# Kernel tuning notes

Measured on AMD Instinct MI355X. Metric: run time of the kernel, lower is better.

## Reference

```python
import jax, jax.numpy as jnp
import numpy as np

N, D, K, P, A = 16384, 256, 32, 64, 5
H, KD, NPT, FACT = 8, 32, 8, 2
RBF_BINS, RBF_MAX, REL_CLIP = 16, 10.0, 32


def _norm(v, eps=1e-6):
    return v * jax.lax.rsqrt(jnp.square(v).sum(-1, keepdims=True) + eps)


def extract_frames(pos):
    # pos: [N, A, 3]; backbone atoms 0=N, 1=CA, 2=C (Gram-Schmidt AF-style frame)
    n, ca, c = pos[:, 0], pos[:, 1], pos[:, 2]
    e1 = _norm(c - ca)
    u = n - ca
    e2 = _norm(u - (u * e1).sum(-1, keepdims=True) * e1)
    e3 = jnp.cross(e1, e2)
    R = jnp.stack([e1, e2, e3], axis=-1)  # [N,3,3], columns = frame axes
    t = ca
    local = jnp.einsum('nji,naj->nai', R, pos - t[:, None])  # R^T (p - t)
    return R, t, local


def distance_rbf(d):
    centers = jnp.linspace(0.0, RBF_MAX, RBF_BINS)
    sigma = RBF_MAX / RBF_BINS
    return jnp.exp(-jnp.square((d[..., None] - centers) / sigma))


def layer_norm(x, scale, offset, eps=1e-5):
    mu = x.mean(-1, keepdims=True)
    var = jnp.square(x - mu).mean(-1, keepdims=True)
    return (x - mu) * jax.lax.rsqrt(var + eps) * scale + offset


def setup_inputs() -> dict:
    key = jax.random.key(0)
    ks = jax.random.split(key, 20)
    f32 = jnp.float32
    rnd = lambda i, shape, s=0.02: jax.random.normal(ks[i], shape, f32) * s
    inp = {}
    inp['local'] = jax.random.normal(ks[0], (N, D), f32)
    inp['pos'] = jax.random.normal(ks[1], (N, A, 3), f32) * 3.0
    inp['neighbours'] = jax.random.randint(ks[2], (N, K), 0, N, jnp.int32)
    inp['resi'] = jnp.arange(N, dtype=jnp.int32) % 512
    inp['chain'] = jnp.arange(N, dtype=jnp.int32) // 2048
    inp['batch'] = jnp.arange(N, dtype=jnp.int32) // 4096
    inp['update_mask'] = jnp.ones((N, 1), bool)
    inp['mask'] = jnp.ones((N,), bool)
    FIN = A * 3 + A * RBF_BINS
    FPAIR = A * 3 + A * RBF_BINS + (2 * REL_CLIP + 1) + 2
    FOUT = H * KD + H * P + H * NPT * 3 + H * NPT
    inp['w_in'] = rnd(3, (FIN, D))
    inp['w_pair'] = rnd(4, (FPAIR, P))
    inp['b_pair'] = jnp.zeros((P,), f32)
    inp['ln1_s'] = jnp.ones((D,), f32); inp['ln1_o'] = jnp.zeros((D,), f32)
    inp['wq'] = rnd(5, (D, H * KD)); inp['wk'] = rnd(6, (D, H * KD)); inp['wv'] = rnd(7, (D, H * KD))
    inp['wqp'] = rnd(8, (D, H * NPT * 3)); inp['wkp'] = rnd(9, (D, H * NPT * 3)); inp['wvp'] = rnd(10, (D, H * NPT * 3))
    inp['wb'] = rnd(11, (P, H))
    inp['gamma'] = jnp.ones((H,), f32)
    inp['wo'] = rnd(12, (FOUT, D)); inp['bo'] = jnp.zeros((D,), f32)
    inp['ln2_s'] = jnp.ones((D,), f32); inp['ln2_o'] = jnp.zeros((D,), f32)
    DH = D * FACT
    inp['wg'] = rnd(13, (D, DH)); inp['wvm'] = rnd(14, (D, DH)); inp['wom'] = rnd(15, (DH, D))
    inp['ln3_s'] = jnp.ones((D,), f32); inp['ln3_o'] = jnp.zeros((D,), f32)
    inp['wpos'] = rnd(16, (D, A * 3))
    return inp


def reference(local, pos, w_in, w_pair, b_pair, ln1_s, ln1_o, wq, wk, wv, wqp, wkp, wvp,
              wb, gamma, wo, bo, ln2_s, ln2_o, wg, wvm, wom, ln3_s, ln3_o, wpos,
              neighbours, resi, chain, batch, update_mask, mask):
    n_res = local.shape[0]
    kk = neighbours.shape[1]
    R, t, local_pos = extract_frames(pos)  # [N,3,3], [N,3], [N,A,3]
    # --- geometric input features ---
    dloc = jnp.sqrt(jnp.square(local_pos).sum(-1) + 1e-12)
    feat = jnp.concatenate([_norm(local_pos).reshape(n_res, -1),
                            distance_rbf(dloc).reshape(n_res, -1)], axis=-1)
    local = local + feat @ w_in
    # --- pair features over kNN edges ---
    idx = jnp.clip(neighbours, 0, n_res - 1)
    pos_j = pos[idx]  # [N,K,A,3]
    rel = jnp.einsum('nji,nkaj->nkai', R, pos_j - t[:, None, None])  # neighbour atoms in frame i
    dij = jnp.sqrt(jnp.square(rel).sum(-1) + 1e-12)  # [N,K,A]
    dirs = rel / (dij[..., None] + 1e-6)
    rp = jnp.clip(resi[idx] - resi[:, None], -REL_CLIP, REL_CLIP) + REL_CLIP
    rp_oh = jax.nn.one_hot(rp, 2 * REL_CLIP + 1, dtype=local.dtype)
    same_chain = (chain[idx] == chain[:, None])[..., None].astype(local.dtype)
    same_batch = (batch[idx] == batch[:, None])[..., None].astype(local.dtype)
    pf = jnp.concatenate([dirs.reshape(n_res, kk, -1), distance_rbf(dij).reshape(n_res, kk, -1),
                          rp_oh, same_chain, same_batch], axis=-1)
    pair = jax.nn.gelu(pf @ w_pair + b_pair)  # [N,K,P]
    pair_mask = mask[:, None] & mask[idx] & (neighbours >= 0) & (batch[idx] == batch[:, None])
    # --- sparse invariant point attention ---
    x = layer_norm(local, ln1_s, ln1_o)
    q = (x @ wq).reshape(n_res, H, KD)
    k = (x @ wk).reshape(n_res, H, KD)
    v = (x @ wv).reshape(n_res, H, KD)
    to_glob = lambda pts: jnp.einsum('nij,nhpj->nhpi', R, pts) + t[:, None, None]
    qp = to_glob((x @ wqp).reshape(n_res, H, NPT, 3))
    kp = to_glob((x @ wkp).reshape(n_res, H, NPT, 3))
    vp = to_glob((x @ wvp).reshape(n_res, H, NPT, 3))
    qk = jnp.einsum('nhd,nkhd->nkh', q, k[idx]) / np.float32(np.sqrt(KD))
    d2 = jnp.square(qp[:, None] - kp[idx]).sum(-1).sum(-1)  # [N,K,H]
    wc = np.float32(np.sqrt(2.0 / (9.0 * NPT)))
    wl = np.float32(np.sqrt(1.0 / 3.0))
    logits = wl * (qk + pair @ wb - 0.5 * wc * jax.nn.softplus(gamma) * d2)
    logits = jnp.where(pair_mask[..., None], logits, -1e9)
    att = jax.nn.softmax(logits, axis=1)
    att = jnp.where(pair_mask[..., None], att, 0.0)
    o_s = jnp.einsum('nkh,nkhd->nhd', att, v[idx]).reshape(n_res, -1)
    o_pt = jnp.einsum('nkh,nkhpi->nhpi', att, vp[idx])
    o_pt = jnp.einsum('nji,nhpj->nhpi', R, o_pt - t[:, None, None])  # back to local frame
    o_n = jnp.sqrt(jnp.square(o_pt).sum(-1) + 1e-8)
    o_pr = jnp.einsum('nkh,nkc->nhc', att, pair).reshape(n_res, -1)
    ipa = jnp.concatenate([o_s, o_pr, o_pt.reshape(n_res, -1), o_n.reshape(n_res, -1)], -1) @ wo + bo
    local = local + ipa
    # --- gated MLP ---
    x = layer_norm(local, ln2_s, ln2_o)
    local = local + (jax.nn.gelu(x @ wg) * (x @ wvm)) @ wom
    # --- equivariant position update (scale = 1.0) ---
    x = layer_norm(local, ln3_s, ln3_o)
    new_lp = local_pos + (x @ wpos).reshape(n_res, A, 3)
    new_pos = jnp.einsum('nij,naj->nai', R, new_lp) + t[:, None]
    pos = jnp.where(update_mask[..., None], new_pos, pos)
    return local, pos
```

## Files before the change

### kernel.cpp

```cpp
#include <hip/hip_runtime.h>
#include <hip/hip_bf16.h>
#include <math.h>

#define DMODEL 256
#define KNB 32
#define NHEAD 8
#define FIN 95
#define FPD 95
#define KPAD 104
#define FOUT 1024
#define DHID 512
#define BTS 36
#define PRS 72

typedef __hip_bfloat16 bf16;
typedef __attribute__((ext_vector_type(8))) short short8;
typedef __attribute__((ext_vector_type(4))) float floatx4;

__device__ inline float B2F(bf16 x) { return __bfloat162float(x); }
__device__ inline bf16 F2B(float x) { return __float2bfloat16(x); }
__device__ inline unsigned short f2bs(float x) {
    bf16 h = __float2bfloat16(x);
    return *reinterpret_cast<unsigned short*>(&h);
}
__device__ inline float bs2f(short s) {
    return __uint_as_float(((unsigned)(unsigned short)s) << 16);
}

__device__ inline float gelu_t(float x) {
    return 0.5f * x * (1.f + tanhf(0.7978845608028654f * (x + 0.044715f * x * x * x)));
}

__device__ inline float gelu_f(float x) {
    float u = 1.5957691216057308f * x * (1.f + 0.044715f * x * x);
    float t = 1.f - 2.f / (1.f + __expf(u));
    return 0.5f * x * (1.f + t);
}

#define OFF_WALL 0
#define OFF_WO   344064
#define OFF_WG   606208
#define OFF_WVM  737280
#define OFF_WOM  868352
#define OFF_WP   999424
#define OFF_WIN  1006080
#define OFF_WBM  1032704
#define WT_TOTAL 1033728

__global__ __launch_bounds__(256) void kT(const float* __restrict__ wq, const float* __restrict__ wk,
                                          const float* __restrict__ wv, const float* __restrict__ wqp,
                                          const float* __restrict__ wkp, const float* __restrict__ wvp,
                                          const float* __restrict__ wo, const float* __restrict__ wg,
                                          const float* __restrict__ wvm, const float* __restrict__ wom,
                                          const float* __restrict__ w_pair, const float* __restrict__ w_in,
                                          const float* __restrict__ wbm,
                                          unsigned short* __restrict__ wt) {
    int stride = gridDim.x * 256;
    for (int e = blockIdx.x * 256 + threadIdx.x; e < WT_TOTAL; e += stride) {
        float v;
        if (e < OFF_WO) {
            int n = e >> 8, k = e & 255;
            if (n < 256) v = wq[k * 256 + n];
            else if (n < 512) v = wk[k * 256 + n - 256];
            else if (n < 768) v = wv[k * 256 + n - 512];
            else if (n < 960) v = wqp[k * 192 + n - 768];
            else if (n < 1152) v = wkp[k * 192 + n - 960];
            else v = wvp[k * 192 + n - 1152];
        } else if (e < OFF_WG) {
            int u = e - OFF_WO; int n = u >> 10, k = u & 1023;
            v = wo[k * 256 + n];
        } else if (e < OFF_WVM) {
            int u = e - OFF_WG; int n = u >> 8, k = u & 255;
            v = wg[k * 512 + n];
        } else if (e < OFF_WOM) {
            int u = e - OFF_WVM; int n = u >> 8, k = u & 255;
            v = wvm[k * 512 + n];
        } else if (e < OFF_WP) {
            int u = e - OFF_WOM; int n = u >> 9, k = u & 511;
            v = wom[k * 256 + n];
        } else if (e < OFF_WIN) {
            int u = e - OFF_WP; int n = u / KPAD, k = u % KPAD;
            v = (k < FPD) ? w_pair[k * 64 + n] : 0.f;
        } else if (e < OFF_WBM) {
            int u = e - OFF_WIN; int n = u / KPAD, k = u % KPAD;
            v = (k < FIN) ? w_in[k * 256 + n] : 0.f;
        } else {
            int u = e - OFF_WBM; int n = u >> 6, k = u & 63;
            v = (n < NHEAD) ? wbm[k * 8 + n] : 0.f;
        }
        wt[e] = f2bs(v);
    }
}

__global__ __launch_bounds__(256) void kA1(const float* __restrict__ pos,
                                           float* __restrict__ Rw,
                                           float* __restrict__ lpw,
                                           unsigned short* __restrict__ featb) {
    int tid = threadIdx.x;
    int res = tid >> 5, lt = tid & 31;
    int ri = blockIdx.x * 8 + res;
    const float* pp = pos + (size_t)ri * 15;
    float nx = pp[0], ny = pp[1], nz = pp[2];
    float cax = pp[3], cay = pp[4], caz = pp[5];
    float cx = pp[6], cy = pp[7], cz = pp[8];
    float e1x = cx - cax, e1y = cy - cay, e1z = cz - caz;
    float inv = rsqrtf(e1x * e1x + e1y * e1y + e1z * e1z + 1e-6f);
    e1x *= inv; e1y *= inv; e1z *= inv;
    float ux = nx - cax, uy = ny - cay, uz = nz - caz;
    float d = ux * e1x + uy * e1y + uz * e1z;
    float wx = ux - d * e1x, wy = uy - d * e1y, wz = uz - d * e1z;
    inv = rsqrtf(wx * wx + wy * wy + wz * wz + 1e-6f);
    float e2x = wx * inv, e2y = wy * inv, e2z = wz * inv;
    float e3x = e1y * e2z - e1z * e2y;
    float e3y = e1z * e2x - e1x * e2z;
    float e3z = e1x * e2y - e1y * e2x;
    float R[9] = {e1x, e2x, e3x, e1y, e2y, e3y, e1z, e2z, e3z};

    __shared__ float lpS[8][15];
    __shared__ float ddS[8][5], dinvS[8][5];

    if (lt < 9) Rw[(size_t)ri * 9 + lt] = R[lt];
    if (lt < 15) {
        int a = lt / 3, ii = lt % 3;
        float px = pp[a * 3 + 0] - cax, py = pp[a * 3 + 1] - cay, pz = pp[a * 3 + 2] - caz;
        float v = R[0 * 3 + ii] * px + R[1 * 3 + ii] * py + R[2 * 3 + ii] * pz;
        lpS[res][lt] = v;
        lpw[(size_t)ri * 15 + lt] = v;
    }
    __syncthreads();
    if (lt < 5) {
        float s = lpS[res][lt * 3] * lpS[res][lt * 3] + lpS[res][lt * 3 + 1] * lpS[res][lt * 3 + 1] +
                  lpS[res][lt * 3 + 2] * lpS[res][lt * 3 + 2];
        ddS[res][lt] = sqrtf(s + 1e-12f);
        dinvS[res][lt] = rsqrtf(s + 1e-6f);
    }
    __syncthreads();
    for (int e = lt; e < KPAD; e += 32) {
        float v;
        if (e < 15) v = lpS[res][e] * dinvS[res][e / 3];
        else if (e < 95) {
            int u = e - 15, a = u >> 4, b = u & 15;
            float z = (ddS[res][a] - (float)b * (10.f / 15.f)) * (1.f / 0.625f);
            v = expf(-z * z);
        } else v = 0.f;
        featb[(size_t)ri * KPAD + e] = f2bs(v);
    }
}

__global__ __launch_bounds__(256) void kB(const float* __restrict__ local,
                                          const unsigned short* __restrict__ featb,
                                          const float* __restrict__ ln1_s,
                                          const float* __restrict__ ln1_o,
                                          const unsigned short* __restrict__ wAllT,
                                          const unsigned short* __restrict__ w_inT,
                                          float* __restrict__ dlocal,
                                          bf16* __restrict__ qbh, bf16* __restrict__ kvb,
                                          bf16* __restrict__ qpl, bf16* __restrict__ kpl,
                                          bf16* __restrict__ vpl) {
    int r0 = blockIdx.x * 32;
    int tid = threadIdx.x;
    __shared__ __align__(16) unsigned short featA[32 * KPAD];
    __shared__ __align__(16) unsigned short xbf[32 * 264];
    __shared__ float statsS[32 * 4];

    {
        const short8* src = reinterpret_cast<const short8*>(featb + (size_t)r0 * KPAD);
        short8* dst = reinterpret_cast<short8*>(featA);
        for (int c = tid; c < 32 * KPAD / 8; c += 256) dst[c] = src[c];
    }
    __syncthreads();

    int lane = tid & 63, w = tid >> 6;
    int mtile = w & 1, par = w >> 1;
    int m = lane & 15, quad = lane >> 4;

    short8 fa[3];
#pragma unroll
    for (int ks = 0; ks < 3; ks++)
        fa[ks] = *reinterpret_cast<const short8*>(&featA[(mtile * 16 + m) * KPAD + ks * 32 + quad * 8]);
    float lupv[8][4];
#pragma unroll
    for (int j = 0; j < 8; j++) {
        int nt = par + 2 * j;
        floatx4 c = {0.f, 0.f, 0.f, 0.f};
        const short8* bp = reinterpret_cast<const short8*>(w_inT + (size_t)(nt * 16 + m) * KPAD);
#pragma unroll
        for (int ks = 0; ks < 3; ks++)
            c = __builtin_amdgcn_mfma_f32_16x16x32_bf16(fa[ks], bp[ks * 4 + quad], c, 0, 0, 0);
        int col = nt * 16 + m;
#pragma unroll
        for (int r = 0; r < 4; r++) {
            int row = mtile * 16 + quad * 4 + r;
            float lv = local[(size_t)(r0 + row) * 256 + col] + c[r];
            lupv[j][r] = lv;
            dlocal[(size_t)(r0 + row) * 256 + col] = lv;
        }
    }
    {
        float s[4] = {0.f, 0.f, 0.f, 0.f}, ss[4] = {0.f, 0.f, 0.f, 0.f};
#pragma unroll
        for (int j = 0; j < 8; j++)
#pragma unroll
            for (int r = 0; r < 4; r++) { s[r] += lupv[j][r]; ss[r] += lupv[j][r] * lupv[j][r]; }
#pragma unroll
        for (int mask = 1; mask < 16; mask <<= 1)
#pragma unroll
            for (int r = 0; r < 4; r++) { s[r] += __shfl_xor(s[r], mask); ss[r] += __shfl_xor(ss[r], mask); }
        if (m == 0) {
#pragma unroll
            for (int r = 0; r < 4; r++) {
                int row = mtile * 16 + quad * 4 + r;
                statsS[row * 4 + par * 2 + 0] = s[r];
                statsS[row * 4 + par * 2 + 1] = ss[r];
            }
        }
    }
    __syncthreads();
    {
        float mu[4], rs_[4];
#pragma unroll
        for (int r = 0; r < 4; r++) {
            int row = mtile * 16 + quad * 4 + r;
            float S = statsS[row * 4 + 0] + statsS[row * 4 + 2];
            float SS = statsS[row * 4 + 1] + statsS[row * 4 + 3];
            float m_ = S * (1.f / 256.f);
            mu[r] = m_;
            rs_[r] = rsqrtf(SS * (1.f / 256.f) - m_ * m_ + 1e-5f);
        }
#pragma unroll
        for (int j = 0; j < 8; j++) {
            int col = (par + 2 * j) * 16 + m;
            float g = ln1_s[col], o = ln1_o[col];
#pragma unroll
            for (int r = 0; r < 4; r++) {
                int row = mtile * 16 + quad * 4 + r;
                xbf[row * 264 + col] = f2bs((lupv[j][r] - mu[r]) * rs_[r] * g + o);
            }
        }
    }
    __syncthreads();

    short8 afr[8];
#pragma unroll
    for (int ks = 0; ks < 8; ks++)
        afr[ks] = *reinterpret_cast<const short8*>(&xbf[(mtile * 16 + m) * 264 + ks * 32 + quad * 8]);
    for (int nt = par; nt < 84; nt += 2) {
        floatx4 c = {0.f, 0.f, 0.f, 0.f};
        const short8* bp = reinterpret_cast<const short8*>(wAllT + (size_t)(nt * 16 + m) * 256);
#pragma unroll
        for (int ks = 0; ks < 8; ks++)
            c = __builtin_amdgcn_mfma_f32_16x16x32_bf16(afr[ks], bp[ks * 4 + quad], c, 0, 0, 0);
        int colg = nt * 16 + m;
        bf16* O; int c0, ncol;
        if (colg < 256)       { O = qbh; c0 = colg;        ncol = 256; }
        else if (colg < 768)  { O = kvb; c0 = colg - 256;  ncol = 512; }
        else if (colg < 960)  { O = qpl; c0 = colg - 768;  ncol = 192; }
        else if (colg < 1152) { O = kpl; c0 = colg - 960;  ncol = 192; }
        else                  { O = vpl; c0 = colg - 1152; ncol = 192; }
#pragma unroll
        for (int r = 0; r < 4; r++) {
            int rg = r0 + mtile * 16 + quad * 4 + r;
            O[(size_t)rg * ncol + c0] = F2B(c[r]);
        }
    }
}

__global__ __launch_bounds__(256) void kP(const bf16* __restrict__ qpl,
                                          const bf16* __restrict__ kpl,
                                          const bf16* __restrict__ vpl,
                                          const float* __restrict__ Rw,
                                          const float* __restrict__ pos,
                                          float* __restrict__ qpg,
                                          float* __restrict__ kvpg) {
    int r0 = blockIdx.x * 4;
    int tid = threadIdx.x;
    for (int u = tid; u < 4 * 192; u += 256) {
        int r = u / 192, e = u % 192, hp = e / 3, ii = e % 3;
        int ri = r0 + r;
        float R0 = Rw[(size_t)ri * 9 + ii * 3 + 0];
        float R1 = Rw[(size_t)ri * 9 + ii * 3 + 1];
        float R2 = Rw[(size_t)ri * 9 + ii * 3 + 2];
        float tt = pos[(size_t)ri * 15 + 3 + ii];
        size_t base = (size_t)ri * 192 + hp * 3;
        qpg[(size_t)ri * 192 + e] = R0 * B2F(qpl[base]) + R1 * B2F(qpl[base + 1]) + R2 * B2F(qpl[base + 2]) + tt;
        kvpg[(size_t)ri * 384 + e] = R0 * B2F(kpl[base]) + R1 * B2F(kpl[base + 1]) + R2 * B2F(kpl[base + 2]) + tt;
        kvpg[(size_t)ri * 384 + 192 + e] = R0 * B2F(vpl[base]) + R1 * B2F(vpl[base + 1]) + R2 * B2F(vpl[base + 2]) + tt;
    }
}

__global__ __launch_bounds__(256) void kC(const float* __restrict__ pos,
                                          const int* __restrict__ nbr,
                                          const int* __restrict__ resi,
                                          const int* __restrict__ chain,
                                          const int* __restrict__ batch,
                                          const int* __restrict__ mask,
                                          const float* __restrict__ Rw,
                                          const float* __restrict__ w_pair,
                                          const unsigned short* __restrict__ wT,
                                          const float* __restrict__ b_pair,
                                          const unsigned short* __restrict__ wbmT,
                                          const float* __restrict__ gamma,
                                          const bf16* __restrict__ qbh,
                                          const bf16* __restrict__ kvb,
                                          const float* __restrict__ qpg,
                                          const float* __restrict__ kvpg,
                                          bf16* __restrict__ ipab,
                                          int N) {
    int i = blockIdx.x;
    int tid = threadIdx.x;
    __shared__ __align__(16) unsigned short BigT[512 * BTS];
    __shared__ __align__(16) unsigned short pairR[32 * PRS];
    __shared__ __align__(16) unsigned short attb[16 * 40];
    __shared__ __align__(16) float qS[256];
    __shared__ __align__(16) float qpS[192];
    __shared__ __align__(16) float pbS[256];
    __shared__ float spS[NHEAD];
    __shared__ int anyS;
    __shared__ int idxS[KNB], rpS[KNB], scS[KNB], sbS[KNB], pmS[KNB];
    __shared__ __align__(16) union UShare {
        unsigned short pfA[32 * KPAD];
        struct { float ipaS[FOUT]; float optg[192]; } o;
    } uS;

    float R[9];
#pragma unroll
    for (int u = 0; u < 9; u++) R[u] = Rw[(size_t)i * 9 + u];
    float t0 = pos[(size_t)i * 15 + 3];
    float t1 = pos[(size_t)i * 15 + 4];
    float t2 = pos[(size_t)i * 15 + 5];

    qS[tid] = B2F(qbh[(size_t)i * 256 + tid]);
    if (tid < 192) qpS[tid] = qpg[(size_t)i * 192 + tid];
    if (tid < NHEAD) spS[tid] = log1pf(expf(gamma[tid]));
    if (tid < KNB) {
        int nb = nbr[(size_t)i * KNB + tid];
        int j = min(max(nb, 0), N - 1);
        idxS[tid] = j;
        int rp = resi[j] - resi[i];
        rp = min(max(rp, -32), 32) + 32;
        rpS[tid] = rp;
        scS[tid] = (chain[j] == chain[i]) ? 1 : 0;
        sbS[tid] = (batch[j] == batch[i]) ? 1 : 0;
        pmS[tid] = (mask[i] != 0 && mask[j] != 0 && nb >= 0 && batch[j] == batch[i]) ? 1 : 0;
    }
    __syncthreads();
    if (tid < 64) {
        unsigned long long b = __ballot((tid < KNB) && (pmS[tid] != 0));
        if (tid == 0) anyS = (b != 0ULL) ? 1 : 0;
    }
    if (tid < 160) {
        int kk = tid & 31, a = tid >> 5;
        int j = idxS[kk];
        const float* pj = pos + (size_t)j * 15 + a * 3;
        float px = pj[0] - t0, py = pj[1] - t1, pz = pj[2] - t2;
        float r0_ = R[0] * px + R[3] * py + R[6] * pz;
        float r1_ = R[1] * px + R[4] * py + R[7] * pz;
        float r2_ = R[2] * px + R[5] * py + R[8] * pz;
        float s = r0_ * r0_ + r1_ * r1_ + r2_ * r2_;
        float dij = sqrtf(s + 1e-12f);
        float di = 1.f / (dij + 1e-6f);
        uS.pfA[kk * KPAD + a * 3 + 0] = f2bs(r0_ * di);
        uS.pfA[kk * KPAD + a * 3 + 1] = f2bs(r1_ * di);
        uS.pfA[kk * KPAD + a * 3 + 2] = f2bs(r2_ * di);
        for (int b = 0; b < 16; b++) {
            float z = (dij - (float)b * (10.f / 15.f)) * (1.f / 0.625f);
            uS.pfA[kk * KPAD + 15 + a * 16 + b] = f2bs(__expf(-z * z));
        }
    }
    if (tid < KNB) uS.pfA[tid * KPAD + FPD] = 0;
    __syncthreads();

    {
        int lane = tid & 63;
        int wv = tid >> 6;
        int n0 = wv * 16;
        int mrow = lane & 15;
        int quad = lane >> 4;
        floatx4 c0 = {0.f, 0.f, 0.f, 0.f};
        floatx4 c1 = {0.f, 0.f, 0.f, 0.f};
#pragma unroll
        for (int ks = 0; ks < 3; ks++) {
            int k0 = ks * 32 + quad * 8;
            short8 a0 = *reinterpret_cast<const short8*>(&uS.pfA[mrow * KPAD + k0]);
            short8 a1 = *reinterpret_cast<const short8*>(&uS.pfA[(16 + mrow) * KPAD + k0]);
            short8 bb = *reinterpret_cast<const short8*>(&wT[(n0 + mrow) * KPAD + k0]);
            c0 = __builtin_amdgcn_mfma_f32_16x16x32_bf16(a0, bb, c0, 0, 0, 0);
            c1 = __builtin_amdgcn_mfma_f32_16x16x32_bf16(a1, bb, c1, 0, 0, 0);
        }
        int col = n0 + mrow;
        float bp = b_pair[col];
        float w160 = w_pair[160 * 64 + col];
        float w161 = w_pair[161 * 64 + col];
#pragma unroll
        for (int mt = 0; mt < 2; mt++) {
            floatx4 cc = mt ? c1 : c0;
#pragma unroll
            for (int r = 0; r < 4; r++) {
                int row = mt * 16 + quad * 4 + r;
                float s = cc[r] + bp + w_pair[(95 + rpS[row]) * 64 + col] +
                          (scS[row] ? w160 : 0.f) + (sbS[row] ? w161 : 0.f);
                unsigned short gb = f2bs(gelu_f(s));
                pairR[row * PRS + col] = gb;
                BigT[(448 + col) * BTS + row] = gb;
            }
        }
    }
    __syncthreads();

    {
        int kk = tid & 31, seg = tid >> 5;
        int j = idxS[kk];
        {
            const short8* src = reinterpret_cast<const short8*>(kvb + (size_t)j * 512 + 256 + seg * 32);
            short8 v0 = src[0], v1 = src[1], v2 = src[2], v3 = src[3];
#pragma unroll
            for (int c = 0; c < 8; c++) BigT[(seg * 32 + c) * BTS + kk] = (unsigned short)v0[c];
#pragma unroll
            for (int c = 0; c < 8; c++) BigT[(seg * 32 + 8 + c) * BTS + kk] = (unsigned short)v1[c];
#pragma unroll
            for (int c = 0; c < 8; c++) BigT[(seg * 32 + 16 + c) * BTS + kk] = (unsigned short)v2[c];
#pragma unroll
            for (int c = 0; c < 8; c++) BigT[(seg * 32 + 24 + c) * BTS + kk] = (unsigned short)v3[c];
        }
        {
            const floatx4* src = reinterpret_cast<const floatx4*>(kvpg + (size_t)j * 384 + 192 + seg * 24);
            floatx4 f[6];
#pragma unroll
            for (int g = 0; g < 6; g++) f[g] = src[g];
            float tv[3] = {t0, t1, t2};
#pragma unroll
            for (int g = 0; g < 6; g++)
#pragma unroll
                for (int c2 = 0; c2 < 4; c2++) {
                    int x = g * 4 + c2;
                    float val = f[g][c2] - tv[x % 3];
                    BigT[(256 + seg * 24 + x) * BTS + kk] = f2bs(val);
                }
        }
    }
    {
        int w = tid >> 6;
        if (w < 2) {
            int lane = tid & 63, la = lane & 15, quad = lane >> 4;
            floatx4 c = {0.f, 0.f, 0.f, 0.f};
#pragma unroll
            for (int ks = 0; ks < 2; ks++) {
                short8 a = *reinterpret_cast<const short8*>(&pairR[(w * 16 + la) * PRS + ks * 32 + quad * 8]);
                short8 b = *reinterpret_cast<const short8*>(wbmT + la * 64 + ks * 32 + quad * 8);
                c = __builtin_amdgcn_mfma_f32_16x16x32_bf16(a, b, c, 0, 0, 0);
            }
            if (la < NHEAD) {
#pragma unroll
                for (int r = 0; r < 4; r++)
                    pbS[(w * 16 + quad * 4 + r) * 8 + la] = c[r];
            }
        }
    }
    __syncthreads();

    {
        int kk = tid >> 3, h = tid & 7;
        int j = idxS[kk];
        float qk = 0.f;
        const short8* kj8 = reinterpret_cast<const short8*>(kvb + (size_t)j * 512 + h * 32);
        const floatx4* qh4 = reinterpret_cast<const floatx4*>(qS + h * 32);
#pragma unroll
        for (int e = 0; e < 4; e++) {
            short8 kv = kj8[e];
            floatx4 qa = qh4[2 * e], qb = qh4[2 * e + 1];
            qk += qa[0] * bs2f(kv[0]) + qa[1] * bs2f(kv[1]) + qa[2] * bs2f(kv[2]) + qa[3] * bs2f(kv[3]) +
                  qb[0] * bs2f(kv[4]) + qb[1] * bs2f(kv[5]) + qb[2] * bs2f(kv[6]) + qb[3] * bs2f(kv[7]);
        }
        qk *= 0.17677669529663687f;
        float d2 = 0.f;
        const floatx4* kp4 = reinterpret_cast<const floatx4*>(kvpg + (size_t)j * 384 + h * 24);
        const floatx4* qp4 = reinterpret_cast<const floatx4*>(qpS + h * 24);
#pragma unroll
        for (int e = 0; e < 6; e++) {
            floatx4 kv = kp4[e], qv = qp4[e];
#pragma unroll
            for (int q = 0; q < 4; q++) {
                float df = qv[q] - kv[q];
                d2 += df * df;
            }
        }
        float pb = pbS[kk * 8 + h];
        float lgt = 0.5773502691896258f * (qk + pb - (1.f / 12.f) * spS[h] * d2);
        pbS[kk * 8 + h] = pmS[kk] ? lgt : -1e9f;
    }
    __syncthreads();

    if (tid < 64) {
        int h = tid >> 3, sub = tid & 7;
        float m = -INFINITY;
        float lv[4];
#pragma unroll
        for (int q = 0; q < 4; q++) {
            lv[q] = pbS[(sub + 8 * q) * 8 + h];
            m = fmaxf(m, lv[q]);
        }
#pragma unroll
        for (int mk = 1; mk < 8; mk <<= 1) m = fmaxf(m, __shfl_xor(m, mk));
        float s = 0.f, ex[4];
#pragma unroll
        for (int q = 0; q < 4; q++) { ex[q] = __expf(lv[q] - m); s += ex[q]; }
#pragma unroll
        for (int mk = 1; mk < 8; mk <<= 1) s += __shfl_xor(s, mk);
        float invs = 1.f / s;
#pragma unroll
        for (int q = 0; q < 4; q++) {
            int kk = sub + 8 * q;
            float a = pmS[kk] ? ex[q] * invs : 0.f;
            attb[h * 40 + kk] = f2bs(a);
        }
    } else if (tid < 128) {
        int t2 = tid - 64;
        int h2 = 8 + (t2 >> 3);
        int k0 = (t2 & 7) * 4;
#pragma unroll
        for (int q = 0; q < 4; q++) attb[h2 * 40 + k0 + q] = 0;
    }
    __syncthreads();

    {
        int lane = tid & 63, w = tid >> 6;
        int la = lane & 15, quad = lane >> 4;
        short8 af = *reinterpret_cast<const short8*>(&attb[la * 40 + quad * 8]);
        float* oB = uS.o.ipaS;
#pragma unroll
        for (int n8 = 0; n8 < 8; n8++) {
            int nt = w * 8 + n8;
            int colg = nt * 16 + la;
            union { short8 s; unsigned long long u[2]; } bb;
            const unsigned long long* bp = reinterpret_cast<const unsigned long long*>(&BigT[colg * BTS + quad * 8]);
            bb.u[0] = bp[0]; bb.u[1] = bp[1];
            floatx4 z = {0.f, 0.f, 0.f, 0.f};
            floatx4 d = __builtin_amdgcn_mfma_f32_16x16x32_bf16(af, bb.s, z, 0, 0, 0);
            if (quad < 2) {
                if (colg < 448) {
                    int h_req, dst;
                    if (colg < 256) { h_req = colg >> 5; dst = (h_req << 5) + (colg & 31); }
                    else            { int e = colg - 256; h_req = e / 24; dst = 1024 + e; }
                    if ((h_req >> 2) == quad) {
#pragma unroll
                        for (int r = 0; r < 4; r++)
                            if ((h_req & 3) == r) oB[dst] = d[r];
                    }
                } else {
                    int c = colg - 448;
#pragma unroll
                    for (int r = 0; r < 4; r++)
                        oB[256 + (quad * 4 + r) * 64 + c] = d[r];
                }
            }
        }
    }
    __syncthreads();

    if (tid < 192) {
        int hp = tid / 3, ii = tid % 3;
        float corr = anyS ? 0.f : -1.f;
        const float* optg = uS.o.ipaS + 1024;
        float v0 = optg[hp * 3 + 0] + corr * t0;
        float v1 = optg[hp * 3 + 1] + corr * t1;
        float v2 = optg[hp * 3 + 2] + corr * t2;
        uS.o.ipaS[768 + tid] = R[0 + ii] * v0 + R[3 + ii] * v1 + R[6 + ii] * v2;
    }
    __syncthreads();
    if (tid < 64) {
        float a0 = uS.o.ipaS[768 + tid * 3], a1 = uS.o.ipaS[768 + tid * 3 + 1], a2 = uS.o.ipaS[768 + tid * 3 + 2];
        uS.o.ipaS[960 + tid] = sqrtf(a0 * a0 + a1 * a1 + a2 * a2 + 1e-8f);
    }
    __syncthreads();
    for (int u = tid; u < FOUT; u += 256) ipab[(size_t)i * FOUT + u] = F2B(uS.o.ipaS[u]);
}

__global__ __launch_bounds__(256) void kDE(const bf16* __restrict__ ipab,
                                           const unsigned short* __restrict__ woT,
                                           const float* __restrict__ bo,
                                           const float* __restrict__ ln2_s,
                                           const float* __restrict__ ln2_o,
                                           const unsigned short* __restrict__ wgT,
                                           const unsigned short* __restrict__ wvmT,
                                           const unsigned short* __restrict__ womT,
                                           float* __restrict__ dlocal) {
    int r0 = blockIdx.x * 32;
    int tid = threadIdx.x;
    __shared__ __align__(16) unsigned short xbf[32 * 264];
    __shared__ __align__(16) unsigned short hbf[32 * 520];
    __shared__ float statsS[32 * 4];
    int lane = tid & 63, w = tid >> 6;
    int mtile = w & 1, par = w >> 1, m = lane & 15, quad = lane >> 4;

    floatx4 l2[8];
#pragma unroll
    for (int j = 0; j < 8; j++) l2[j] = {0.f, 0.f, 0.f, 0.f};
    const short8* arow = reinterpret_cast<const short8*>(ipab + (size_t)(r0 + mtile * 16 + m) * 1024);
    for (int ks = 0; ks < 32; ks++) {
        short8 a = arow[ks * 4 + quad];
#pragma unroll
        for (int j = 0; j < 8; j++) {
            int nt = par + 2 * j;
            const short8* bp = reinterpret_cast<const short8*>(woT + (size_t)(nt * 16 + m) * 1024);
            l2[j] = __builtin_amdgcn_mfma_f32_16x16x32_bf16(a, bp[ks * 4 + quad], l2[j], 0, 0, 0);
        }
    }
#pragma unroll
    for (int j = 0; j < 8; j++) {
        int colg = (par + 2 * j) * 16 + m;
        float bov = bo[colg];
#pragma unroll
        for (int r = 0; r < 4; r++) {
            int row = mtile * 16 + quad * 4 + r;
            l2[j][r] += dlocal[(size_t)(r0 + row) * 256 + colg] + bov;
        }
    }
    {
        float s[4] = {0.f, 0.f, 0.f, 0.f}, ss[4] = {0.f, 0.f, 0.f, 0.f};
#pragma unroll
        for (int j = 0; j < 8; j++)
#pragma unroll
            for (int r = 0; r < 4; r++) { s[r] += l2[j][r]; ss[r] += l2[j][r] * l2[j][r]; }
#pragma unroll
        for (int mask = 1; mask < 16; mask <<= 1)
#pragma unroll
            for (int r = 0; r < 4; r++) { s[r] += __shfl_xor(s[r], mask); ss[r] += __shfl_xor(ss[r], mask); }
        if (m == 0) {
#pragma unroll
            for (int r = 0; r < 4; r++) {
                int row = mtile * 16 + quad * 4 + r;
                statsS[row * 4 + par * 2 + 0] = s[r];
                statsS[row * 4 + par * 2 + 1] = ss[r];
            }
        }
    }
    __syncthreads();
    {
        float mu[4], rs_[4];
#pragma unroll
        for (int r = 0; r < 4; r++) {
            int row = mtile * 16 + quad * 4 + r;
            float S = statsS[row * 4 + 0] + statsS[row * 4 + 2];
            float SS = statsS[row * 4 + 1] + statsS[row * 4 + 3];
            float m_ = S * (1.f / 256.f);
            mu[r] = m_;
            rs_[r] = rsqrtf(SS * (1.f / 256.f) - m_ * m_ + 1e-5f);
        }
#pragma unroll
        for (int j = 0; j < 8; j++) {
            int colg = (par + 2 * j) * 16 + m;
            float g = ln2_s[colg], o = ln2_o[colg];
#pragma unroll
            for (int r = 0; r < 4; r++) {
                int row = mtile * 16 + quad * 4 + r;
                xbf[row * 264 + colg] = f2bs((l2[j][r] - mu[r]) * rs_[r] * g + o);
            }
        }
    }
    __syncthreads();
    short8 afr[8];
#pragma unroll
    for (int ks = 0; ks < 8; ks++)
        afr[ks] = *reinterpret_cast<const short8*>(&xbf[(mtile * 16 + m) * 264 + ks * 32 + quad * 8]);
    for (int nt = par; nt < 32; nt += 2) {
        floatx4 cg = {0.f, 0.f, 0.f, 0.f};
        floatx4 cv = {0.f, 0.f, 0.f, 0.f};
        const short8* bg = reinterpret_cast<const short8*>(wgT + (size_t)(nt * 16 + m) * 256);
        const short8* bv = reinterpret_cast<const short8*>(wvmT + (size_t)(nt * 16 + m) * 256);
#pragma unroll
        for (int ks = 0; ks < 8; ks++) {
            cg = __builtin_amdgcn_mfma_f32_16x16x32_bf16(afr[ks], bg[ks * 4 + quad], cg, 0, 0, 0);
            cv = __builtin_amdgcn_mfma_f32_16x16x32_bf16(afr[ks], bv[ks * 4 + quad], cv, 0, 0, 0);
        }
#pragma unroll
        for (int r = 0; r < 4; r++) {
            int row = mtile * 16 + quad * 4 + r;
            hbf[row * 520 + nt * 16 + m] = f2bs(gelu_t(cg[r]) * cv[r]);
        }
    }
    __syncthreads();
    floatx4 acc[8];
#pragma unroll
    for (int j = 0; j < 8; j++) acc[j] = {0.f, 0.f, 0.f, 0.f};
    for (int ks = 0; ks < 16; ks++) {
        short8 a = *reinterpret_cast<const short8*>(&hbf[(mtile * 16 + m) * 520 + ks * 32 + quad * 8]);
#pragma unroll
        for (int j = 0; j < 8; j++) {
            int nt = par + 2 * j;
            const short8* bp = reinterpret_cast<const short8*>(womT + (size_t)(nt * 16 + m) * 512);
            acc[j] = __builtin_amdgcn_mfma_f32_16x16x32_bf16(a, bp[ks * 4 + quad], acc[j], 0, 0, 0);
        }
    }
#pragma unroll
    for (int j = 0; j < 8; j++) {
        int colg = (par + 2 * j) * 16 + m;
#pragma unroll
        for (int r = 0; r < 4; r++) {
            int row = mtile * 16 + quad * 4 + r;
            dlocal[(size_t)(r0 + row) * 256 + colg] = l2[j][r] + acc[j][r];
        }
    }
}

__global__ __launch_bounds__(256) void kF(const float* __restrict__ dlocal,
                                          const float* __restrict__ ln3_s,
                                          const float* __restrict__ ln3_o,
                                          const float* __restrict__ wpos,
                                          const float* __restrict__ lpw,
                                          const float* __restrict__ Rw,
                                          const float* __restrict__ pos,
                                          const int* __restrict__ umask,
                                          float* __restrict__ outp) {
    int tid = threadIdx.x;
    int r = tid >> 5, lt = tid & 31;
    int ri = blockIdx.x * 8 + r;
    __shared__ float x3S[8][256];
    __shared__ float nlS[8][15];
    {
        const floatx4* src = reinterpret_cast<const floatx4*>(dlocal + (size_t)ri * 256 + lt * 8);
        floatx4 v0 = src[0], v1 = src[1];
        float s = 0.f, ss = 0.f;
#pragma unroll
        for (int q = 0; q < 4; q++) {
            s += v0[q] + v1[q];
            ss += v0[q] * v0[q] + v1[q] * v1[q];
        }
#pragma unroll
        for (int mask = 1; mask < 32; mask <<= 1) { s += __shfl_xor(s, mask); ss += __shfl_xor(ss, mask); }
        float mu = s * (1.f / 256.f);
        float var = ss * (1.f / 256.f) - mu * mu;
        float rs = rsqrtf(var + 1e-5f);
#pragma unroll
        for (int q = 0; q < 4; q++) {
            int f0 = lt * 8 + q, f1 = lt * 8 + 4 + q;
            x3S[r][f0] = (v0[q] - mu) * rs * ln3_s[f0] + ln3_o[f0];
            x3S[r][f1] = (v1[q] - mu) * rs * ln3_s[f1] + ln3_o[f1];
        }
    }
    __syncthreads();
    {
        int g = tid >> 5, sub = tid & 31;
        for (int out = g; out < 120; out += 8) {
            int rr = out / 15, e = out % 15;
            float partial = 0.f;
#pragma unroll
            for (int i2 = 0; i2 < 8; i2++) {
                int f = sub + 32 * i2;
                partial += x3S[rr][f] * wpos[f * 15 + e];
            }
#pragma unroll
            for (int mask = 1; mask < 32; mask <<= 1) partial += __shfl_xor(partial, mask);
            if (sub == 0) nlS[rr][e] = lpw[(size_t)(blockIdx.x * 8 + rr) * 15 + e] + partial;
        }
    }
    __syncthreads();
    if (tid < 120) {
        int rr = tid / 15, e = tid % 15;
        int rj = blockIdx.x * 8 + rr;
        int a2 = e / 3, ii = e % 3;
        float R0 = Rw[(size_t)rj * 9 + ii * 3 + 0];
        float R1 = Rw[(size_t)rj * 9 + ii * 3 + 1];
        float R2 = Rw[(size_t)rj * 9 + ii * 3 + 2];
        float tt = pos[(size_t)rj * 15 + 3 + ii];
        float np = R0 * nlS[rr][a2 * 3 + 0] + R1 * nlS[rr][a2 * 3 + 1] + R2 * nlS[rr][a2 * 3 + 2] + tt;
        float old = pos[(size_t)rj * 15 + e];
        outp[(size_t)rj * 15 + e] = (umask[rj] != 0) ? np : old;
    }
}

extern "C" void kernel_launch(void* const* d_in, const int* in_sizes, int n_in,
                              void* d_out, int out_size, void* d_ws, size_t ws_size,
                              hipStream_t stream) {
    static const int map_dict[31] = {0, 1, 2, 3, 4, 5, 6, 7, 8, 9, 10, 11, 12, 13, 14, 15,
                                     16, 17, 18, 19, 20, 21, 22, 23, 24, 25, 26, 27, 28, 29, 30};
    static const int map_sig[31] = {0, 1, 25, 26, 27, 28, 29, 30, 2, 3, 4, 5, 6, 7, 8, 9,
                                    10, 11, 12, 13, 14, 15, 16, 17, 18, 19, 20, 21, 22, 23, 24};
    const int* M = (in_sizes[2] == FIN * DMODEL) ? map_sig : map_dict;

    const float* local = (const float*)d_in[M[0]];
    const float* pos = (const float*)d_in[M[1]];
    const int* nbr = (const int*)d_in[M[2]];
    const int* resi = (const int*)d_in[M[3]];
    const int* chain = (const int*)d_in[M[4]];
    const int* batch = (const int*)d_in[M[5]];
    const int* umask = (const int*)d_in[M[6]];
    const int* mask = (const int*)d_in[M[7]];
    const float* w_in = (const float*)d_in[M[8]];
    const float* w_pair = (const float*)d_in[M[9]];
    const float* b_pair = (const float*)d_in[M[10]];
    const float* ln1_s = (const float*)d_in[M[11]];
    const float* ln1_o = (const float*)d_in[M[12]];
    const float* wq = (const float*)d_in[M[13]];
    const float* wk = (const float*)d_in[M[14]];
    const float* wv = (const float*)d_in[M[15]];
    const float* wqp = (const float*)d_in[M[16]];
    const float* wkp = (const float*)d_in[M[17]];
    const float* wvp = (const float*)d_in[M[18]];
    const float* wbm = (const float*)d_in[M[19]];
    const float* gamma = (const float*)d_in[M[20]];
    const float* wo = (const float*)d_in[M[21]];
    const float* bo = (const float*)d_in[M[22]];
    const float* ln2_s = (const float*)d_in[M[23]];
    const float* ln2_o = (const float*)d_in[M[24]];
    const float* wg = (const float*)d_in[M[25]];
    const float* wvm = (const float*)d_in[M[26]];
    const float* wom = (const float*)d_in[M[27]];
    const float* ln3_s = (const float*)d_in[M[28]];
    const float* ln3_o = (const float*)d_in[M[29]];
    const float* wpos = (const float*)d_in[M[30]];

    int N = in_sizes[0] / DMODEL;

    float* out_local = (float*)d_out;
    float* out_pos = out_local + (size_t)N * DMODEL;

    char* wsb = (char*)d_ws;
    float* Rw = (float*)wsb;   wsb += (size_t)N * 9 * 4;
    float* lpw = (float*)wsb;  wsb += (size_t)N * 15 * 4;
    bf16* qbh = (bf16*)wsb;    wsb += (size_t)N * 256 * 2;
    bf16* kvb = (bf16*)wsb;    wsb += (size_t)N * 512 * 2;
    bf16* qpl = (bf16*)wsb;    wsb += (size_t)N * 192 * 2;
    bf16* kpl = (bf16*)wsb;    wsb += (size_t)N * 192 * 2;
    bf16* vpl = (bf16*)wsb;    wsb += (size_t)N * 192 * 2;
    bf16* ipab = (bf16*)wsb;   wsb += (size_t)N * 1024 * 2;
    float* qpg = (float*)wsb;  wsb += (size_t)N * 192 * 4;
    float* kvpg = (float*)wsb; wsb += (size_t)N * 384 * 4;
    unsigned short* featb = (unsigned short*)wsb; wsb += (size_t)N * KPAD * 2;
    unsigned short* wtrans = (unsigned short*)wsb; wsb += (size_t)WT_TOTAL * 2;
    unsigned short* wAllT = wtrans + OFF_WALL;
    unsigned short* woT   = wtrans + OFF_WO;
    unsigned short* wgT   = wtrans + OFF_WG;
    unsigned short* wvmT  = wtrans + OFF_WVM;
    unsigned short* womT  = wtrans + OFF_WOM;
    unsigned short* wpT   = wtrans + OFF_WP;
    unsigned short* winT  = wtrans + OFF_WIN;
    unsigned short* wbmT  = wtrans + OFF_WBM;

    dim3 blk(256);
    hipLaunchKernelGGL(kT, dim3(512), blk, 0, stream, wq, wk, wv, wqp, wkp, wvp,
                       wo, wg, wvm, wom, w_pair, w_in, wbm, wtrans);
    hipLaunchKernelGGL(kA1, dim3(N / 8), blk, 0, stream, pos, Rw, lpw, featb);
    hipLaunchKernelGGL(kB, dim3(N / 32), blk, 0, stream, local, featb, ln1_s, ln1_o, wAllT, winT,
                       out_local, qbh, kvb, qpl, kpl, vpl);
    hipLaunchKernelGGL(kP, dim3(N / 4), blk, 0, stream, qpl, kpl, vpl, Rw, pos, qpg, kvpg);
    hipLaunchKernelGGL(kC, dim3(N), blk, 0, stream, pos, nbr, resi, chain, batch, mask, Rw,
                       w_pair, wpT, b_pair, wbmT, gamma, qbh, kvb, qpg, kvpg, ipab, N);
    hipLaunchKernelGGL(kDE, dim3(N / 32), blk, 0, stream, ipab, woT, bo, ln2_s, ln2_o,
                       wgT, wvmT, womT, out_local);
    hipLaunchKernelGGL(kF, dim3(N / 8), blk, 0, stream, out_local, ln3_s, ln3_o, wpos, lpw, Rw, pos,
                       umask, out_pos);
}
```

Baseline: 702.7 us.

## Store neighbour key/value points as untranslated bf16 and prefetch gathers early in kC

kP now writes key/value points in bf16 without the translation term, halving that buffer. kC adds the neighbour translation back algebraically, through tjS in the distance term and an attention-weighted sum attjS in the output points. kC also issues its neighbour gathers of V, value points, K and key points into registers early so the load latency overlaps the pair-feature work. Fast exp and the exp-based GELU replace expf and tanh. The cost is lower precision on the point coordinates and higher register pressure from the prefetched vectors.

```diff
diff --git a/kernel.cpp b/kernel.cpp
--- a/kernel.cpp
+++ b/kernel.cpp
@@ -25,10 +25,6 @@
 }
 __device__ inline float bs2f(short s) {
     return __uint_as_float(((unsigned)(unsigned short)s) << 16);
-}
-
-__device__ inline float gelu_t(float x) {
-    return 0.5f * x * (1.f + tanhf(0.7978845608028654f * (x + 0.044715f * x * x * x)));
 }
 
 __device__ inline float gelu_f(float x) {
@@ -141,7 +137,7 @@
         else if (e < 95) {
             int u = e - 15, a = u >> 4, b = u & 15;
             float z = (ddS[res][a] - (float)b * (10.f / 15.f)) * (1.f / 0.625f);
-            v = expf(-z * z);
+            v = __expf(-z * z);
         } else v = 0.f;
         featb[(size_t)ri * KPAD + e] = f2bs(v);
     }
@@ -271,7 +267,7 @@
                                           const float* __restrict__ Rw,
                                           const float* __restrict__ pos,
                                           float* __restrict__ qpg,
-                                          float* __restrict__ kvpg) {
+                                          bf16* __restrict__ kvpgh) {
     int r0 = blockIdx.x * 4;
     int tid = threadIdx.x;
     for (int u = tid; u < 4 * 192; u += 256) {
@@ -283,8 +279,8 @@
         float tt = pos[(size_t)ri * 15 + 3 + ii];
         size_t base = (size_t)ri * 192 + hp * 3;
         qpg[(size_t)ri * 192 + e] = R0 * B2F(qpl[base]) + R1 * B2F(qpl[base + 1]) + R2 * B2F(qpl[base + 2]) + tt;
-        kvpg[(size_t)ri * 384 + e] = R0 * B2F(kpl[base]) + R1 * B2F(kpl[base + 1]) + R2 * B2F(kpl[base + 2]) + tt;
-        kvpg[(size_t)ri * 384 + 192 + e] = R0 * B2F(vpl[base]) + R1 * B2F(vpl[base + 1]) + R2 * B2F(vpl[base + 2]) + tt;
+        kvpgh[(size_t)ri * 384 + e] = F2B(R0 * B2F(kpl[base]) + R1 * B2F(kpl[base + 1]) + R2 * B2F(kpl[base + 2]));
+        kvpgh[(size_t)ri * 384 + 192 + e] = F2B(R0 * B2F(vpl[base]) + R1 * B2F(vpl[base + 1]) + R2 * B2F(vpl[base + 2]));
     }
 }
 
@@ -303,7 +299,7 @@
                                           const bf16* __restrict__ qbh,
                                           const bf16* __restrict__ kvb,
                                           const float* __restrict__ qpg,
-                                          const float* __restrict__ kvpg,
+                                          const bf16* __restrict__ kvpgh,
                                           bf16* __restrict__ ipab,
                                           int N) {
     int i = blockIdx.x;
@@ -315,13 +311,29 @@
     __shared__ __align__(16) float qpS[192];
     __shared__ __align__(16) float pbS[256];
     __shared__ float spS[NHEAD];
-    __shared__ int anyS;
+    __shared__ float tjS[KNB][3];
+    __shared__ float attjS[24];
     __shared__ int idxS[KNB], rpS[KNB], scS[KNB], sbS[KNB], pmS[KNB];
     __shared__ __align__(16) union UShare {
         unsigned short pfA[32 * KPAD];
         struct { float ipaS[FOUT]; float optg[192]; } o;
     } uS;
 
+    int kk_s = tid & 31, seg = tid >> 5;
+    int jpre;
+    {
+        int nb = nbr[(size_t)i * KNB + kk_s];
+        jpre = min(max(nb, 0), N - 1);
+    }
+    short8 pv0, pv1, pv2, pv3, pp0, pp1, pp2;
+    {
+        const short8* vsrc = reinterpret_cast<const short8*>(kvb + (size_t)jpre * 512 + 256 + seg * 32);
+        pv0 = vsrc[0]; pv1 = vsrc[1]; pv2 = vsrc[2]; pv3 = vsrc[3];
+        const unsigned short* vpb = reinterpret_cast<const unsigned short*>(kvpgh) + (size_t)jpre * 384 + 192 + seg * 24;
+        const short8* vpsrc = reinterpret_cast<const short8*>(vpb);
+        pp0 = vpsrc[0]; pp1 = vpsrc[1]; pp2 = vpsrc[2];
+    }
+
     float R[9];
 #pragma unroll
     for (int u = 0; u < 9; u++) R[u] = Rw[(size_t)i * 9 + u];
@@ -331,7 +343,7 @@
 
     qS[tid] = B2F(qbh[(size_t)i * 256 + tid]);
     if (tid < 192) qpS[tid] = qpg[(size_t)i * 192 + tid];
-    if (tid < NHEAD) spS[tid] = log1pf(expf(gamma[tid]));
+    if (tid < NHEAD) spS[tid] = log1pf(__expf(gamma[tid]));
     if (tid < KNB) {
         int nb = nbr[(size_t)i * KNB + tid];
         int j = min(max(nb, 0), N - 1);
@@ -344,15 +356,13 @@
         pmS[tid] = (mask[i] != 0 && mask[j] != 0 && nb >= 0 && batch[j] == batch[i]) ? 1 : 0;
     }
     __syncthreads();
-    if (tid < 64) {
-        unsigned long long b = __ballot((tid < KNB) && (pmS[tid] != 0));
-        if (tid == 0) anyS = (b != 0ULL) ? 1 : 0;
-    }
     if (tid < 160) {
         int kk = tid & 31, a = tid >> 5;
         int j = idxS[kk];
         const float* pj = pos + (size_t)j * 15 + a * 3;
-        float px = pj[0] - t0, py = pj[1] - t1, pz = pj[2] - t2;
+        float pj0 = pj[0], pj1 = pj[1], pj2 = pj[2];
+        if (a == 1) { tjS[kk][0] = pj0; tjS[kk][1] = pj1; tjS[kk][2] = pj2; }
+        float px = pj0 - t0, py = pj1 - t1, pz = pj2 - t2;
         float r0_ = R[0] * px + R[3] * py + R[6] * pz;
         float r1_ = R[1] * px + R[4] * py + R[7] * pz;
         float r2_ = R[2] * px + R[5] * py + R[8] * pz;
@@ -407,36 +417,32 @@
     }
     __syncthreads();
 
-    {
-        int kk = tid & 31, seg = tid >> 5;
-        int j = idxS[kk];
-        {
-            const short8* src = reinterpret_cast<const short8*>(kvb + (size_t)j * 512 + 256 + seg * 32);
-            short8 v0 = src[0], v1 = src[1], v2 = src[2], v3 = src[3];
-#pragma unroll
-            for (int c = 0; c < 8; c++) BigT[(seg * 32 + c) * BTS + kk] = (unsigned short)v0[c];
-#pragma unroll
-            for (int c = 0; c < 8; c++) BigT[(seg * 32 + 8 + c) * BTS + kk] = (unsigned short)v1[c];
-#pragma unroll
-            for (int c = 0; c < 8; c++) BigT[(seg * 32 + 16 + c) * BTS + kk] = (unsigned short)v2[c];
-#pragma unroll
-            for (int c = 0; c < 8; c++) BigT[(seg * 32 + 24 + c) * BTS + kk] = (unsigned short)v3[c];
-        }
-        {
-            const floatx4* src = reinterpret_cast<const floatx4*>(kvpg + (size_t)j * 384 + 192 + seg * 24);
-            floatx4 f[6];
-#pragma unroll
-            for (int g = 0; g < 6; g++) f[g] = src[g];
-            float tv[3] = {t0, t1, t2};
-#pragma unroll
-            for (int g = 0; g < 6; g++)
-#pragma unroll
-                for (int c2 = 0; c2 < 4; c2++) {
-                    int x = g * 4 + c2;
-                    float val = f[g][c2] - tv[x % 3];
-                    BigT[(256 + seg * 24 + x) * BTS + kk] = f2bs(val);
-                }
-        }
+    short8 pk0, pk1, pk2, pk3, pq0, pq1, pq2;
+    {
+        int kk2 = tid >> 3, h2 = tid & 7;
+        int j2 = idxS[kk2];
+        const short8* ksrc = reinterpret_cast<const short8*>(kvb + (size_t)j2 * 512 + h2 * 32);
+        pk0 = ksrc[0]; pk1 = ksrc[1]; pk2 = ksrc[2]; pk3 = ksrc[3];
+        const unsigned short* kpb = reinterpret_cast<const unsigned short*>(kvpgh) + (size_t)j2 * 384 + h2 * 24;
+        const short8* kpsrc = reinterpret_cast<const short8*>(kpb);
+        pq0 = kpsrc[0]; pq1 = kpsrc[1]; pq2 = kpsrc[2];
+    }
+    {
+        int kk = kk_s;
+#pragma unroll
+        for (int c = 0; c < 8; c++) BigT[(seg * 32 + c) * BTS + kk] = (unsigned short)pv0[c];
+#pragma unroll
+        for (int c = 0; c < 8; c++) BigT[(seg * 32 + 8 + c) * BTS + kk] = (unsigned short)pv1[c];
+#pragma unroll
+        for (int c = 0; c < 8; c++) BigT[(seg * 32 + 16 + c) * BTS + kk] = (unsigned short)pv2[c];
+#pragma unroll
+        for (int c = 0; c < 8; c++) BigT[(seg * 32 + 24 + c) * BTS + kk] = (unsigned short)pv3[c];
+#pragma unroll
+        for (int c = 0; c < 8; c++) BigT[(256 + seg * 24 + c) * BTS + kk] = (unsigned short)pp0[c];
+#pragma unroll
+        for (int c = 0; c < 8; c++) BigT[(256 + seg * 24 + 8 + c) * BTS + kk] = (unsigned short)pp1[c];
+#pragma unroll
+        for (int c = 0; c < 8; c++) BigT[(256 + seg * 24 + 16 + c) * BTS + kk] = (unsigned short)pp2[c];
     }
     {
         int w = tid >> 6;
@@ -460,30 +466,29 @@
 
     {
         int kk = tid >> 3, h = tid & 7;
-        int j = idxS[kk];
         float qk = 0.f;
-        const short8* kj8 = reinterpret_cast<const short8*>(kvb + (size_t)j * 512 + h * 32);
         const floatx4* qh4 = reinterpret_cast<const floatx4*>(qS + h * 32);
+        short8 kvv[4] = {pk0, pk1, pk2, pk3};
 #pragma unroll
         for (int e = 0; e < 4; e++) {
-            short8 kv = kj8[e];
+            short8 kv = kvv[e];
             floatx4 qa = qh4[2 * e], qb = qh4[2 * e + 1];
             qk += qa[0] * bs2f(kv[0]) + qa[1] * bs2f(kv[1]) + qa[2] * bs2f(kv[2]) + qa[3] * bs2f(kv[3]) +
                   qb[0] * bs2f(kv[4]) + qb[1] * bs2f(kv[5]) + qb[2] * bs2f(kv[6]) + qb[3] * bs2f(kv[7]);
         }
         qk *= 0.17677669529663687f;
         float d2 = 0.f;
-        const floatx4* kp4 = reinterpret_cast<const floatx4*>(kvpg + (size_t)j * 384 + h * 24);
-        const floatx4* qp4 = reinterpret_cast<const floatx4*>(qpS + h * 24);
-#pragma unroll
-        for (int e = 0; e < 6; e++) {
-            floatx4 kv = kp4[e], qv = qp4[e];
-#pragma unroll
-            for (int q = 0; q < 4; q++) {
-                float df = qv[q] - kv[q];
+        const float* qp = qpS + h * 24;
+        float tj[3] = {tjS[kk][0], tjS[kk][1], tjS[kk][2]};
+        short8 kpv[3] = {pq0, pq1, pq2};
+#pragma unroll
+        for (int e8 = 0; e8 < 3; e8++)
+#pragma unroll
+            for (int c8 = 0; c8 < 8; c8++) {
+                int x = e8 * 8 + c8;
+                float df = (qp[x] - tj[x % 3]) - bs2f(kpv[e8][c8]);
                 d2 += df * df;
             }
-        }
         float pb = pbS[kk * 8 + h];
         float lgt = 0.5773502691896258f * (qk + pb - (1.f / 12.f) * spS[h] * d2);
         pbS[kk * 8 + h] = pmS[kk] ? lgt : -1e9f;
@@ -512,6 +517,7 @@
             int kk = sub + 8 * q;
             float a = pmS[kk] ? ex[q] * invs : 0.f;
             attb[h * 40 + kk] = f2bs(a);
+            pbS[kk * 8 + h] = a;
         }
     } else if (tid < 128) {
         int t2 = tid - 64;
@@ -555,15 +561,22 @@
             }
         }
     }
+    if (tid < 24) {
+        int h = tid / 3, c = tid % 3;
+        float s = 0.f;
+#pragma unroll
+        for (int kk = 0; kk < KNB; kk++) s += pbS[kk * 8 + h] * tjS[kk][c];
+        attjS[tid] = s;
+    }
     __syncthreads();
 
     if (tid < 192) {
         int hp = tid / 3, ii = tid % 3;
-        float corr = anyS ? 0.f : -1.f;
+        int h = hp >> 3;
         const float* optg = uS.o.ipaS + 1024;
-        float v0 = optg[hp * 3 + 0] + corr * t0;
-        float v1 = optg[hp * 3 + 1] + corr * t1;
-        float v2 = optg[hp * 3 + 2] + corr * t2;
+        float v0 = optg[hp * 3 + 0] + attjS[h * 3 + 0] - t0;
+        float v1 = optg[hp * 3 + 1] + attjS[h * 3 + 1] - t1;
+        float v2 = optg[hp * 3 + 2] + attjS[h * 3 + 2] - t2;
         uS.o.ipaS[768 + tid] = R[0 + ii] * v0 + R[3 + ii] * v1 + R[6 + ii] * v2;
     }
     __syncthreads();
@@ -675,7 +688,7 @@
 #pragma unroll
         for (int r = 0; r < 4; r++) {
             int row = mtile * 16 + quad * 4 + r;
-            hbf[row * 520 + nt * 16 + m] = f2bs(gelu_t(cg[r]) * cv[r]);
+            hbf[row * 520 + nt * 16 + m] = f2bs(gelu_f(cg[r]) * cv[r]);
         }
     }
     __syncthreads();
@@ -824,7 +837,7 @@
     bf16* vpl = (bf16*)wsb;    wsb += (size_t)N * 192 * 2;
     bf16* ipab = (bf16*)wsb;   wsb += (size_t)N * 1024 * 2;
     float* qpg = (float*)wsb;  wsb += (size_t)N * 192 * 4;
-    float* kvpg = (float*)wsb; wsb += (size_t)N * 384 * 4;
+    bf16* kvpgh = (bf16*)wsb;  wsb += (size_t)N * 384 * 2;
     unsigned short* featb = (unsigned short*)wsb; wsb += (size_t)N * KPAD * 2;
     unsigned short* wtrans = (unsigned short*)wsb; wsb += (size_t)WT_TOTAL * 2;
     unsigned short* wAllT = wtrans + OFF_WALL;
@@ -842,9 +855,9 @@
     hipLaunchKernelGGL(kA1, dim3(N / 8), blk, 0, stream, pos, Rw, lpw, featb);
     hipLaunchKernelGGL(kB, dim3(N / 32), blk, 0, stream, local, featb, ln1_s, ln1_o, wAllT, winT,
                        out_local, qbh, kvb, qpl, kpl, vpl);
-    hipLaunchKernelGGL(kP, dim3(N / 4), blk, 0, stream, qpl, kpl, vpl, Rw, pos, qpg, kvpg);
+    hipLaunchKernelGGL(kP, dim3(N / 4), blk, 0, stream, qpl, kpl, vpl, Rw, pos, qpg, kvpgh);
     hipLaunchKernelGGL(kC, dim3(N), blk, 0, stream, pos, nbr, resi, chain, batch, mask, Rw,
-                       w_pair, wpT, b_pair, wbmT, gamma, qbh, kvb, qpg, kvpg, ipab, N);
+                       w_pair, wpT, b_pair, wbmT, gamma, qbh, kvb, qpg, kvpgh, ipab, N);
     hipLaunchKernelGGL(kDE, dim3(N / 32), blk, 0, stream, ipab, woT, bo, ln2_s, ln2_o,
                        wgT, wvmT, womT, out_local);
     hipLaunchKernelGGL(kF, dim3(N / 8), blk, 0, stream, out_local, ln3_s, ln3_o, wpos, lpw, Rw, pos,
```

After: 680.1 us. 3.2% less time.
